# Kernel optimization log

Measured on AMD Instinct MI355X. Metric: run time of the kernel, lower is better.

Reference implementation:

```python
import jax, jax.numpy as jnp
import numpy as np

N, M, E = 20000, 2000, 320000
D_MODEL, HID, HEADS = 128, 128, 4
EPS_BN = 1e-5


def _seg_softmax(a, seg, n):
    # torch_geometric.utils.softmax grouped by seg (here: destination node)
    m = jax.ops.segment_max(a, seg, num_segments=n)
    e = jnp.exp(a - m[seg])
    s = jax.ops.segment_sum(e, seg, num_segments=n)
    return e / (s[seg] + 1e-16)


def _bn(x, g, b):
    # BatchNorm1d, training-mode batch statistics (biased var), affine
    mu = x.mean(0)
    v = x.var(0)
    return (x - mu) * jax.lax.rsqrt(v + EPS_BN) * g + b


def _hconv(x, attr, node_idx, edge_idx, w_edge, lin_w, att, bias, heads):
    # PyG HypergraphConv(use_attention=True, concat=False), dropout off (eval)
    nN, nM = x.shape[0], w_edge.shape[0]
    C = lin_w.shape[1] // heads
    xh = (x @ lin_w).reshape(nN, heads, C)      # node feats per head
    ah = (attr @ lin_w).reshape(nM, heads, C)   # hyperedge feats per head
    x_i = xh[node_idx]                          # [E,H,C] gather per incidence
    a_j = ah[edge_idx]                          # [E,H,C]
    alpha = (x_i * att[:, :C]).sum(-1) + (a_j * att[:, C:]).sum(-1)  # [E,H]
    alpha = jax.nn.leaky_relu(alpha, 0.2)
    alpha = _seg_softmax(alpha, node_idx, nN)
    # D = sum of incident hyperedge weights per node; B = 1/edge_degree * w
    Dd = jax.ops.segment_sum(w_edge[edge_idx], node_idx, num_segments=nN)
    Dinv = jnp.where(Dd > 0, 1.0 / Dd, 0.0)
    Bd = jax.ops.segment_sum(jnp.ones((node_idx.shape[0],), x.dtype), edge_idx, num_segments=nM)
    Binv = jnp.where(Bd > 0, 1.0 / Bd, 0.0) * w_edge
    # node -> hyperedge
    m1 = Binv[edge_idx][:, None, None] * alpha[:, :, None] * x_i
    out_e = jax.ops.segment_sum(m1, edge_idx, num_segments=nM)  # [M,H,C]
    # hyperedge -> node
    m2 = Dinv[node_idx][:, None, None] * alpha[:, :, None] * out_e[edge_idx]
    out_n = jax.ops.segment_sum(m2, node_idx, num_segments=nN)  # [N,H,C]
    return out_n.mean(axis=1) + bias            # concat=False -> head mean


def _forward(x, node_idx, edge_idx, hyperedge_weight, W1, b1, g1, be1,
             lin_w1, att1, bias1, g2, be2, lin_w2, att2, bias2, g3, be3,
             W2, b2, g4, be4):
    nM = hyperedge_weight.shape[0]
    src = x
    h = jax.nn.leaky_relu(x @ W1 + b1, 0.2)
    h = _bn(h, g1, be1)
    # hyperedge_attr = (a.T @ x) == segment_sum of node feats per hyperedge
    attr = jax.ops.segment_sum(h[node_idx], edge_idx, num_segments=nM)
    h = _bn(h + _hconv(h, attr, node_idx, edge_idx, hyperedge_weight,
                       lin_w1, att1, bias1, HEADS), g2, be2)
    attr = jax.ops.segment_sum(h[node_idx], edge_idx, num_segments=nM)
    h = _bn(h + _hconv(h, attr, node_idx, edge_idx, hyperedge_weight,
                       lin_w2, att2, bias2, 1), g3, be3)
    o = jax.nn.leaky_relu(h @ W2 + b2, 0.2)
    return _bn(src + o, g4, be4)


def setup_inputs() -> dict:
    key = jax.random.key(0)
    ks = jax.random.split(key, 12)
    s1 = 1.0 / np.sqrt(D_MODEL)
    s2 = 1.0 / np.sqrt(HID)
    return {
        "x": jax.random.normal(ks[0], (N, D_MODEL), jnp.float32),
        "node_idx": jax.random.randint(ks[1], (E,), 0, N),
        "edge_idx": jax.random.randint(ks[2], (E,), 0, M),
        "hyperedge_weight": jax.random.uniform(ks[3], (M,), jnp.float32, 0.5, 1.5),
        "W1": jax.random.normal(ks[4], (D_MODEL, HID), jnp.float32) * s1,
        "b1": jnp.zeros((HID,), jnp.float32),
        "g1": jnp.ones((HID,), jnp.float32),
        "be1": jnp.zeros((HID,), jnp.float32),
        "lin_w1": jax.random.normal(ks[5], (HID, HEADS * HID), jnp.float32) * s2,
        "att1": jax.random.normal(ks[6], (HEADS, 2 * HID), jnp.float32) * s2,
        "bias1": jnp.zeros((HID,), jnp.float32),
        "g2": jnp.ones((HID,), jnp.float32),
        "be2": jnp.zeros((HID,), jnp.float32),
        "lin_w2": jax.random.normal(ks[7], (HID, HID), jnp.float32) * s2,
        "att2": jax.random.normal(ks[8], (1, 2 * HID), jnp.float32) * s2,
        "bias2": jnp.zeros((HID,), jnp.float32),
        "g3": jnp.ones((HID,), jnp.float32),
        "be3": jnp.zeros((HID,), jnp.float32),
        "W2": jax.random.normal(ks[9], (HID, D_MODEL), jnp.float32) * s2,
        "b2": jnp.zeros((D_MODEL,), jnp.float32),
        "g4": jnp.ones((D_MODEL,), jnp.float32),
        "be4": jnp.zeros((D_MODEL,), jnp.float32),
    }


def reference(x, node_idx, edge_idx, hyperedge_weight, W1, b1, g1, be1,
              lin_w1, att1, bias1, g2, be2, lin_w2, att2, bias2, g3, be3,
              W2, b2, g4, be4):
    return _forward(x, node_idx, edge_idx, hyperedge_weight, W1, b1, g1, be1,
                    lin_w1, att1, bias1, g2, be2, lin_w2, att2, bias2,
                    g3, be3, W2, b2, g4, be4)
```

## Files before the change

### kernel.cpp

```cpp
#include <hip/hip_runtime.h>

#define NN 20000
#define MM 2000
#define EE 320000
static constexpr float SLOPE = 0.2f;
static constexpr float EPSBN = 1e-5f;

__device__ inline float4 f4add(float4 a, float4 b) {
  return make_float4(a.x + b.x, a.y + b.y, a.z + b.z, a.w + b.w);
}
__device__ inline float4 f4fma(float a, float4 v, float4 c) {
  return make_float4(c.x + a * v.x, c.y + a * v.y, c.z + a * v.z, c.w + a * v.w);
}
__device__ inline float leaky(float v) { return (v > 0.f) ? v : SLOPE * v; }

__device__ inline void bn_sc4(const float* __restrict__ st, const float* __restrict__ g,
                              const float* __restrict__ be, float ninv, int c4,
                              float4& sc, float4& sh) {
  float* scp = &sc.x;
  float* shp = &sh.x;
#pragma unroll
  for (int j = 0; j < 4; j++) {
    int c = c4 * 4 + j;
    float mu = st[c] * ninv;
    float var = st[128 + c] * ninv - mu * mu;
    float s = g[c] * rsqrtf(var + EPSBN);
    scp[j] = s;
    shp[j] = be[c] - mu * s;
  }
}

__global__ void k_count(const int* __restrict__ ni, const int* __restrict__ ei,
                        int* ncnt, int* ecnt, int* __restrict__ rank_n,
                        int* __restrict__ rank_e) {
  int e = blockIdx.x * 256 + threadIdx.x;
  if (e >= EE) return;
  rank_n[e] = atomicAdd(&ncnt[ni[e]], 1);
  rank_e[e] = atomicAdd(&ecnt[ei[e]], 1);
}

__global__ __launch_bounds__(1024) void k_scan(const int* __restrict__ cnt,
                                               int* __restrict__ off, int n) {
  __shared__ int swav[16];
  __shared__ int sCarry;
  int t = threadIdx.x;
  int lane = t & 63, wid = t >> 6;
  if (t == 0) sCarry = 0;
  __syncthreads();
  for (int base = 0; base < n; base += 1024) {
    int i = base + t;
    int v = (i < n) ? cnt[i] : 0;
    int x = v;
#pragma unroll
    for (int o = 1; o < 64; o <<= 1) {
      int y = __shfl_up(x, o);
      if (lane >= o) x += y;
    }
    if (lane == 63) swav[wid] = x;
    __syncthreads();
    if (wid == 0) {
      int s = (lane < 16) ? swav[lane] : 0;
#pragma unroll
      for (int o = 1; o < 16; o <<= 1) {
        int y = __shfl_up(s, o);
        if (lane >= o) s += y;
      }
      if (lane < 16) swav[lane] = s;
    }
    __syncthreads();
    int wpre = wid ? swav[wid - 1] : 0;
    int total = swav[15];
    if (i < n) off[i] = sCarry + wpre + x - v;
    __syncthreads();
    if (t == 0) sCarry += total;
    __syncthreads();
  }
  if (t == 0) off[n] = sCarry;
}

__global__ void k_fill(const int* __restrict__ ni, const int* __restrict__ ei,
                       const int* __restrict__ noff, const int* __restrict__ eoff,
                       const int* __restrict__ rank_n, const int* __restrict__ rank_e,
                       int* __restrict__ em_n, int2* __restrict__ npos_e) {
  int e = blockIdx.x * 256 + threadIdx.x;
  if (e >= EE) return;
  int n = ni[e];
  int m = ei[e];
  int pn = noff[n] + rank_n[e];
  int pe = eoff[m] + rank_e[e];
  em_n[pn] = m;
  npos_e[pe] = make_int2(n, pn);
}

__global__ __launch_bounds__(256) void k_gemm128(
    const float* __restrict__ A, const float* __restrict__ W,
    const float* __restrict__ bias, const float* __restrict__ resid,
    const float* __restrict__ st, const float* __restrict__ g,
    const float* __restrict__ be, float ninv, float* __restrict__ out,
    float* __restrict__ stout, int rows) {
  __shared__ float As[32][68];
  __shared__ float Ws[32][132];
  __shared__ float scs[128], shs[128];
  if (st && threadIdx.x < 128) {
    int c = threadIdx.x;
    float mu = st[c] * ninv;
    float var = st[128 + c] * ninv - mu * mu;
    float s = g[c] * rsqrtf(var + EPSBN);
    scs[c] = s;
    shs[c] = be[c] - mu * s;
  }
  if (st) __syncthreads();
  int tx = threadIdx.x & 15, ty = threadIdx.x >> 4;
  int r0 = blockIdx.x * 64;
  float4 acc[4][2];
#pragma unroll
  for (int j = 0; j < 4; j++) acc[j][0] = acc[j][1] = make_float4(0.f, 0.f, 0.f, 0.f);

  for (int k0 = 0; k0 < 128; k0 += 32) {
    __syncthreads();
    {
      int row = threadIdx.x >> 2, kq = threadIdx.x & 3;
      int rr = r0 + row;
      float4 a0 = make_float4(0.f, 0.f, 0.f, 0.f), a1 = a0;
      if (rr < rows) {
        const float* ap = A + (size_t)rr * 128 + k0 + kq * 8;
        a0 = ((const float4*)ap)[0];
        a1 = ((const float4*)ap)[1];
      }
      int kb = k0 + kq * 8;
      if (st) {
        a0.x = a0.x * scs[kb + 0] + shs[kb + 0];
        a0.y = a0.y * scs[kb + 1] + shs[kb + 1];
        a0.z = a0.z * scs[kb + 2] + shs[kb + 2];
        a0.w = a0.w * scs[kb + 3] + shs[kb + 3];
        a1.x = a1.x * scs[kb + 4] + shs[kb + 4];
        a1.y = a1.y * scs[kb + 5] + shs[kb + 5];
        a1.z = a1.z * scs[kb + 6] + shs[kb + 6];
        a1.w = a1.w * scs[kb + 7] + shs[kb + 7];
      }
      int kl = kq * 8;
      As[kl + 0][row] = a0.x;
      As[kl + 1][row] = a0.y;
      As[kl + 2][row] = a0.z;
      As[kl + 3][row] = a0.w;
      As[kl + 4][row] = a1.x;
      As[kl + 5][row] = a1.y;
      As[kl + 6][row] = a1.z;
      As[kl + 7][row] = a1.w;
    }
    {
      int kk = threadIdx.x >> 3, cq = threadIdx.x & 7;
      const float* wp = W + (size_t)(k0 + kk) * 128 + cq * 16;
#pragma unroll
      for (int f = 0; f < 4; f++)
        *(float4*)&Ws[kk][cq * 16 + f * 4] = ((const float4*)wp)[f];
    }
    __syncthreads();
#pragma unroll
    for (int kk = 0; kk < 32; kk++) {
      float4 a = *(const float4*)&As[kk][ty * 4];
      float4 w0 = *(const float4*)&Ws[kk][tx * 8];
      float4 w1 = *(const float4*)&Ws[kk][tx * 8 + 4];
      acc[0][0] = f4fma(a.x, w0, acc[0][0]);
      acc[0][1] = f4fma(a.x, w1, acc[0][1]);
      acc[1][0] = f4fma(a.y, w0, acc[1][0]);
      acc[1][1] = f4fma(a.y, w1, acc[1][1]);
      acc[2][0] = f4fma(a.z, w0, acc[2][0]);
      acc[2][1] = f4fma(a.z, w1, acc[2][1]);
      acc[3][0] = f4fma(a.w, w0, acc[3][0]);
      acc[3][1] = f4fma(a.w, w1, acc[3][1]);
    }
  }
  float4 b0 = ((const float4*)bias)[tx * 2];
  float4 b1 = ((const float4*)bias)[tx * 2 + 1];
  float4 cs0 = make_float4(0.f, 0.f, 0.f, 0.f), cs1 = cs0, cq0 = cs0, cq1 = cs0;
#pragma unroll
  for (int j = 0; j < 4; j++) {
    int r = r0 + ty * 4 + j;
    if (r < rows) {
      float4 o0 = acc[j][0], o1 = acc[j][1];
      o0 = make_float4(leaky(o0.x + b0.x), leaky(o0.y + b0.y), leaky(o0.z + b0.z),
                       leaky(o0.w + b0.w));
      o1 = make_float4(leaky(o1.x + b1.x), leaky(o1.y + b1.y), leaky(o1.z + b1.z),
                       leaky(o1.w + b1.w));
      if (resid) {
        float4 r0v = ((const float4*)resid)[(size_t)r * 32 + tx * 2];
        float4 r1v = ((const float4*)resid)[(size_t)r * 32 + tx * 2 + 1];
        o0 = f4add(o0, r0v);
        o1 = f4add(o1, r1v);
      }
      ((float4*)out)[(size_t)r * 32 + tx * 2] = o0;
      ((float4*)out)[(size_t)r * 32 + tx * 2 + 1] = o1;
      cs0 = f4add(cs0, o0);
      cs1 = f4add(cs1, o1);
      cq0 = make_float4(cq0.x + o0.x * o0.x, cq0.y + o0.y * o0.y, cq0.z + o0.z * o0.z,
                        cq0.w + o0.w * o0.w);
      cq1 = make_float4(cq1.x + o1.x * o1.x, cq1.y + o1.y * o1.y, cq1.z + o1.z * o1.z,
                        cq1.w + o1.w * o1.w);
    }
  }
  __syncthreads();
  float* sumb = &As[0][0];
  float* sqb = &Ws[0][0];
  *(float4*)&sumb[ty * 128 + tx * 8] = cs0;
  *(float4*)&sumb[ty * 128 + tx * 8 + 4] = cs1;
  *(float4*)&sqb[ty * 128 + tx * 8] = cq0;
  *(float4*)&sqb[ty * 128 + tx * 8 + 4] = cq1;
  __syncthreads();
  if (threadIdx.x < 128) {
    float S = 0.f, Q = 0.f;
#pragma unroll
    for (int w = 0; w < 16; w++) {
      S += sumb[w * 128 + threadIdx.x];
      Q += sqb[w * 128 + threadIdx.x];
    }
    atomicAdd(&stout[threadIdx.x], S);
    atomicAdd(&stout[128 + threadIdx.x], Q);
  }
}

template <int H>
__global__ __launch_bounds__(256) void k_oute64(const float* __restrict__ T,
                                                const float* __restrict__ linw,
                                                const int* __restrict__ eoff,
                                                const float* __restrict__ wedge,
                                                float* __restrict__ oute) {
  int h = blockIdx.y;
  __shared__ float As[32][68];
  __shared__ float Ws[32][132];
  int tx = threadIdx.x & 15, ty = threadIdx.x >> 4;
  int r0 = blockIdx.x * 64;
  const float* A = T + (size_t)h * MM * 128;
  float4 acc[4][2];
#pragma unroll
  for (int j = 0; j < 4; j++) acc[j][0] = acc[j][1] = make_float4(0.f, 0.f, 0.f, 0.f);

  for (int k0 = 0; k0 < 128; k0 += 32) {
    __syncthreads();
    {
      int row = threadIdx.x >> 2, kq = threadIdx.x & 3;
      int rr = r0 + row;
      float4 a0 = make_float4(0.f, 0.f, 0.f, 0.f), a1 = a0;
      if (rr < MM) {
        const float* ap = A + (size_t)rr * 128 + k0 + kq * 8;
        a0 = ((const float4*)ap)[0];
        a1 = ((const float4*)ap)[1];
      }
      int kb = kq * 8;
      As[kb + 0][row] = a0.x;
      As[kb + 1][row] = a0.y;
      As[kb + 2][row] = a0.z;
      As[kb + 3][row] = a0.w;
      As[kb + 4][row] = a1.x;
      As[kb + 5][row] = a1.y;
      As[kb + 6][row] = a1.z;
      As[kb + 7][row] = a1.w;
    }
    {
      int kk = threadIdx.x >> 3, cq = threadIdx.x & 7;
      const float* wp = linw + (size_t)(k0 + kk) * (128 * H) + h * 128 + cq * 16;
#pragma unroll
      for (int f = 0; f < 4; f++)
        *(float4*)&Ws[kk][cq * 16 + f * 4] = ((const float4*)wp)[f];
    }
    __syncthreads();
#pragma unroll
    for (int kk = 0; kk < 32; kk++) {
      float4 a = *(const float4*)&As[kk][ty * 4];
      float4 w0 = *(const float4*)&Ws[kk][tx * 8];
      float4 w1 = *(const float4*)&Ws[kk][tx * 8 + 4];
      acc[0][0] = f4fma(a.x, w0, acc[0][0]);
      acc[0][1] = f4fma(a.x, w1, acc[0][1]);
      acc[1][0] = f4fma(a.y, w0, acc[1][0]);
      acc[1][1] = f4fma(a.y, w1, acc[1][1]);
      acc[2][0] = f4fma(a.z, w0, acc[2][0]);
      acc[2][1] = f4fma(a.z, w1, acc[2][1]);
      acc[3][0] = f4fma(a.w, w0, acc[3][0]);
      acc[3][1] = f4fma(a.w, w1, acc[3][1]);
    }
  }
#pragma unroll
  for (int j = 0; j < 4; j++) {
    int m = r0 + ty * 4 + j;
    if (m >= MM) break;
    int d = eoff[m + 1] - eoff[m];
    float bv = (d > 0) ? wedge[m] / (float)d : 0.f;
    float4 o0 = acc[j][0], o1 = acc[j][1];
    o0 = make_float4(bv * o0.x, bv * o0.y, bv * o0.z, bv * o0.w);
    o1 = make_float4(bv * o1.x, bv * o1.y, bv * o1.z, bv * o1.w);
    ((float4*)oute)[((size_t)m * H + h) * 32 + tx * 2] = o0;
    ((float4*)oute)[((size_t)m * H + h) * 32 + tx * 2 + 1] = o1;
  }
}

__global__ __launch_bounds__(256) void k_colstats(const float4* __restrict__ X4,
                                                  int rows, float* __restrict__ st) {
  int c4 = threadIdx.x & 31, rs = threadIdx.x >> 5, wid = threadIdx.x >> 6;
  int r0 = blockIdx.x * 256;
  int rend = min(r0 + 256, rows);
  float4 s = make_float4(0.f, 0.f, 0.f, 0.f), q = s;
  for (int r = r0 + rs; r < rend; r += 8) {
    float4 v = X4[(size_t)r * 32 + c4];
    s = f4add(s, v);
    q = make_float4(q.x + v.x * v.x, q.y + v.y * v.y, q.z + v.z * v.z, q.w + v.w * v.w);
  }
  s.x += __shfl_xor(s.x, 32); s.y += __shfl_xor(s.y, 32);
  s.z += __shfl_xor(s.z, 32); s.w += __shfl_xor(s.w, 32);
  q.x += __shfl_xor(q.x, 32); q.y += __shfl_xor(q.y, 32);
  q.z += __shfl_xor(q.z, 32); q.w += __shfl_xor(q.w, 32);
  __shared__ float4 red[4][32][2];
  if ((threadIdx.x & 63) < 32) {
    red[wid][c4][0] = s;
    red[wid][c4][1] = q;
  }
  __syncthreads();
  if (threadIdx.x < 32) {
    float4 S = f4add(f4add(red[0][threadIdx.x][0], red[1][threadIdx.x][0]),
                     f4add(red[2][threadIdx.x][0], red[3][threadIdx.x][0]));
    float4 Q = f4add(f4add(red[0][threadIdx.x][1], red[1][threadIdx.x][1]),
                     f4add(red[2][threadIdx.x][1], red[3][threadIdx.x][1]));
    int c = threadIdx.x * 4;
    atomicAdd(&st[c + 0], S.x);
    atomicAdd(&st[c + 1], S.y);
    atomicAdd(&st[c + 2], S.z);
    atomicAdd(&st[c + 3], S.w);
    atomicAdd(&st[128 + c + 0], Q.x);
    atomicAdd(&st[128 + c + 1], Q.y);
    atomicAdd(&st[128 + c + 2], Q.z);
    atomicAdd(&st[128 + c + 3], Q.w);
  }
}

__global__ void k_bnapply_final(const float4* __restrict__ X4,
                                const float* __restrict__ st,
                                const float* __restrict__ g,
                                const float* __restrict__ be, float ninv,
                                float4* __restrict__ Y4, int total4) {
  int i = blockIdx.x * 256 + threadIdx.x;
  if (i >= total4) return;
  int c4 = i & 31;
  float4 sc, sh;
  bn_sc4(st, g, be, ninv, c4, sc, sh);
  float4 v = X4[i];
  Y4[i] = make_float4(v.x * sc.x + sh.x, v.y * sc.y + sh.y, v.z * sc.z + sh.z,
                      v.w * sc.w + sh.w);
}

template <int H>
__global__ void k_uv(const float* __restrict__ linw, const float* __restrict__ att,
                     float* __restrict__ UVT) {
  int idx = blockIdx.x * 256 + threadIdx.x;
  if (idx >= 128 * H) return;
  int h = idx >> 7, k = idx & 127;
  float u = 0.f, v = 0.f;
  for (int c = 0; c < 128; c++) {
    float w = linw[(size_t)k * (128 * H) + h * 128 + c];
    u += w * att[h * 256 + c];
    v += w * att[h * 256 + 128 + c];
  }
  UVT[h * 128 + k] = u;
  UVT[(H + h) * 128 + k] = v;
}

template <int H>
__global__ void k_dots(const float4* __restrict__ X4, int rows,
                       const float* __restrict__ UVT, const float* __restrict__ st,
                       const float* __restrict__ g, const float* __restrict__ be,
                       float ninv, float* __restrict__ dotx, float* __restrict__ hv) {
  __shared__ float4 Ut[2 * H * 32];
  __shared__ float4 scl[32], shl[32];
  if (threadIdx.x < 32) {
    float4 sc, sh;
    bn_sc4(st, g, be, ninv, threadIdx.x, sc, sh);
    scl[threadIdx.x] = sc;
    shl[threadIdx.x] = sh;
  }
  for (int i = threadIdx.x; i < 2 * H * 32; i += 256) Ut[i] = ((const float4*)UVT)[i];
  __syncthreads();
  int idx = blockIdx.x * 256 + threadIdx.x;
  if (idx >= rows * 2 * H) return;
  int n = idx / (2 * H), h2 = idx - n * (2 * H);
  const float4* xr = X4 + (size_t)n * 32;
  const float4* ur = Ut + h2 * 32;
  float s = 0.f;
#pragma unroll 8
  for (int q = 0; q < 32; q++) {
    float4 a = xr[q], b = ur[q], c = scl[q], d = shl[q];
    float ax = a.x * c.x + d.x, ay = a.y * c.y + d.y;
    float az = a.z * c.z + d.z, aw = a.w * c.w + d.w;
    s += ax * b.x + ay * b.y + az * b.z + aw * b.w;
  }
  if (h2 < H)
    dotx[n * H + h2] = s;
  else
    hv[n * H + (h2 - H)] = s;
}

template <int H>
__global__ void k_dota(const float* __restrict__ hv, const int* __restrict__ eoff,
                       const int2* __restrict__ npos_e, float* __restrict__ dota) {
  int lane = threadIdx.x & 63;
  int m = blockIdx.x * 4 + (threadIdx.x >> 6);
  int s = eoff[m], t = eoff[m + 1];
  if (H == 4) {
    float4 acc = make_float4(0.f, 0.f, 0.f, 0.f);
    const float4* hv4 = (const float4*)hv;
    for (int j = s + lane; j < t; j += 64) acc = f4add(acc, hv4[npos_e[j].x]);
#pragma unroll
    for (int o = 32; o >= 1; o >>= 1) {
      acc.x += __shfl_xor(acc.x, o);
      acc.y += __shfl_xor(acc.y, o);
      acc.z += __shfl_xor(acc.z, o);
      acc.w += __shfl_xor(acc.w, o);
    }
    if (lane == 0) ((float4*)dota)[m] = acc;
  } else {
    float acc = 0.f;
    for (int j = s + lane; j < t; j += 64) acc += hv[npos_e[j].x];
#pragma unroll
    for (int o = 32; o >= 1; o >>= 1) acc += __shfl_xor(acc, o);
    if (lane == 0) dota[m] = acc;
  }
}

template <int H>
__global__ void k_softmax(const int* __restrict__ noff, const int* __restrict__ em_n,
                          const float* __restrict__ dotx, const float* __restrict__ dota,
                          const float* __restrict__ wedge, float* __restrict__ alpha,
                          float* __restrict__ Dinv) {
  int lane = threadIdx.x & 63;
  int n = blockIdx.x * 4 + (threadIdx.x >> 6);
  int s = noff[n], t = noff[n + 1];
  int deg = t - s;
  int h = lane & (H - 1);
  float dx = dotx[n * H + h];
  if (deg <= 64) {
    int em0 = 0;
    float dd = 0.f;
    if (lane < deg) {
      em0 = em_n[s + lane];
      dd = wedge[em0];
    }
#pragma unroll
    for (int o = 32; o >= 1; o >>= 1) dd += __shfl_xor(dd, o);
    if (lane == 0) Dinv[n] = (dd > 0.f) ? 1.f / dd : 0.f;

    constexpr int KMAX = (H == 4) ? 4 : 1;
    int P = deg * H;
    float vc[KMAX];
    float mx = -3.0e38f;
#pragma unroll
    for (int k = 0; k < KMAX; k++) {
      int p = lane + 64 * k;
      int idx = (H == 4) ? (p >> 2) : p;
      int em = __shfl(em0, idx);
      float v = dx + dota[em * H + h];
      v = leaky(v);
      vc[k] = v;
      if (p < P) mx = fmaxf(mx, v);
    }
#pragma unroll
    for (int o = H; o < 64; o <<= 1) mx = fmaxf(mx, __shfl_xor(mx, o));
    float sm = 0.f;
#pragma unroll
    for (int k = 0; k < KMAX; k++) {
      int p = lane + 64 * k;
      float e = __expf(vc[k] - mx);
      vc[k] = e;
      if (p < P) sm += e;
    }
#pragma unroll
    for (int o = H; o < 64; o <<= 1) sm += __shfl_xor(sm, o);
    float inv = 1.f / (sm + 1e-16f);
#pragma unroll
    for (int k = 0; k < KMAX; k++) {
      int p = lane + 64 * k;
      if (p < P) alpha[s * H + p] = vc[k] * inv;
    }
  } else {
    float dd = 0.f;
    for (int i = s + lane; i < t; i += 64) dd += wedge[em_n[i]];
#pragma unroll
    for (int o = 32; o >= 1; o >>= 1) dd += __shfl_xor(dd, o);
    if (lane == 0) Dinv[n] = (dd > 0.f) ? 1.f / dd : 0.f;
    int P = deg * H;
    float mx = -3.0e38f;
    for (int p = lane; p < P; p += 64) {
      int i = s + ((H == 4) ? (p >> 2) : p);
      float v = leaky(dx + dota[em_n[i] * H + h]);
      mx = fmaxf(mx, v);
    }
#pragma unroll
    for (int o = H; o < 64; o <<= 1) mx = fmaxf(mx, __shfl_xor(mx, o));
    float sm = 0.f;
    for (int p = lane; p < P; p += 64) {
      int i = s + ((H == 4) ? (p >> 2) : p);
      float v = leaky(dx + dota[em_n[i] * H + h]);
      sm += __expf(v - mx);
    }
#pragma unroll
    for (int o = H; o < 64; o <<= 1) sm += __shfl_xor(sm, o);
    float inv = 1.f / (sm + 1e-16f);
    for (int p = lane; p < P; p += 64) {
      int i = s + ((H == 4) ? (p >> 2) : p);
      float v = leaky(dx + dota[em_n[i] * H + h]);
      alpha[s * H + p] = __expf(v - mx) * inv;
    }
  }
}

template <int H>
__global__ __launch_bounds__(256) void k_T(const float4* __restrict__ h4raw,
                                           const int* __restrict__ eoff,
                                           const int2* __restrict__ npos_e,
                                           const float* __restrict__ alpha,
                                           const float* __restrict__ st,
                                           const float* __restrict__ g,
                                           const float* __restrict__ be, float ninv,
                                           float4* __restrict__ T4) {
  int m = blockIdx.x;
  int slot = threadIdx.x >> 5, c = threadIdx.x & 31;
  int wv = threadIdx.x >> 6;
  int s = eoff[m], t = eoff[m + 1];
  __shared__ int sofs[256];
  __shared__ float sal[256 * H];
  __shared__ float4 red[4][H][32];
  __shared__ float4 redA[4];
  __shared__ float sAsum[4];
  float4 acc[H];
#pragma unroll
  for (int hh = 0; hh < H; hh++) acc[hh] = make_float4(0.f, 0.f, 0.f, 0.f);
  float4 asum = make_float4(0.f, 0.f, 0.f, 0.f);

  for (int c0 = s; c0 < t; c0 += 256) {
    int cnt = min(256, t - c0);
    __syncthreads();
    if (threadIdx.x < cnt) {
      int2 np = npos_e[c0 + threadIdx.x];
      sofs[threadIdx.x] = np.x * 32;
      if (H == 4) {
        float4 a4 = ((const float4*)alpha)[np.y];
        ((float4*)sal)[threadIdx.x] = a4;
        asum = f4add(asum, a4);
      } else {
        float a = alpha[np.y];
        sal[threadIdx.x] = a;
        asum.x += a;
      }
    }
    __syncthreads();
#pragma unroll 4
    for (int j = slot; j < cnt; j += 8) {
      int ofs = sofs[j];
      float4 v = h4raw[(size_t)ofs + c];
      if (H == 4) {
        float4 a4 = ((const float4*)sal)[j];
        acc[0] = f4fma(a4.x, v, acc[0]);
        acc[1 % H] = f4fma(a4.y, v, acc[1 % H]);
        acc[2 % H] = f4fma(a4.z, v, acc[2 % H]);
        acc[3 % H] = f4fma(a4.w, v, acc[3 % H]);
      } else {
        acc[0] = f4fma(sal[j], v, acc[0]);
      }
    }
  }
#pragma unroll
  for (int hh = 0; hh < H; hh++) {
    float4 a = acc[hh];
    a.x += __shfl_xor(a.x, 32); a.y += __shfl_xor(a.y, 32);
    a.z += __shfl_xor(a.z, 32); a.w += __shfl_xor(a.w, 32);
    acc[hh] = a;
  }
#pragma unroll
  for (int o = 32; o >= 1; o >>= 1) {
    asum.x += __shfl_xor(asum.x, o); asum.y += __shfl_xor(asum.y, o);
    asum.z += __shfl_xor(asum.z, o); asum.w += __shfl_xor(asum.w, o);
  }
  if ((threadIdx.x & 63) < 32) {
#pragma unroll
    for (int hh = 0; hh < H; hh++) red[wv][hh][c] = acc[hh];
  }
  if ((threadIdx.x & 63) == 0) redA[wv] = asum;
  __syncthreads();
  if (threadIdx.x == 0) {
    float4 A = f4add(f4add(redA[0], redA[1]), f4add(redA[2], redA[3]));
    sAsum[0] = A.x; sAsum[1] = A.y; sAsum[2] = A.z; sAsum[3] = A.w;
  }
  __syncthreads();
  if (threadIdx.x < 32 * H) {
    int hh = threadIdx.x >> 5, cc = threadIdx.x & 31;
    float4 r = f4add(f4add(red[0][hh][cc], red[1][hh][cc]),
                     f4add(red[2][hh][cc], red[3][hh][cc]));
    float as = sAsum[hh];
    float4 sc, sh;
    bn_sc4(st, g, be, ninv, cc, sc, sh);
    r = make_float4(sc.x * r.x + sh.x * as, sc.y * r.y + sh.y * as,
                    sc.z * r.z + sh.z * as, sc.w * r.w + sh.w * as);
    T4[((size_t)hh * MM + m) * 32 + cc] = r;
  }
}

template <int H>
__global__ __launch_bounds__(256) void k_phase9(
    const int* __restrict__ noff, const int* __restrict__ em_n,
    const float* __restrict__ alpha, const float4* __restrict__ oute4,
    const float* __restrict__ Dinv, const float* __restrict__ bias,
    const float4* __restrict__ hres4, const float* __restrict__ st,
    const float* __restrict__ g, const float* __restrict__ be, float ninv,
    float4* __restrict__ out4) {
  int wv = threadIdx.x >> 6, lane = threadIdx.x & 63;
  int n = blockIdx.x * 4 + wv;
  int slot = lane >> 5, c = lane & 31;
  int s = noff[n], t = noff[n + 1];
  int deg = t - s;
  float4 acc = make_float4(0.f, 0.f, 0.f, 0.f);
  if (deg <= 64) {
    int m_l = 0;
    float4 a_l = make_float4(0.f, 0.f, 0.f, 0.f);
    if (lane < deg) {
      m_l = em_n[s + lane];
      if (H == 4)
        a_l = ((const float4*)alpha)[s + lane];
      else
        a_l.x = alpha[s + lane];
    }
    for (int i = slot; i < deg; i += 2) {
      int m = __shfl(m_l, i);
      if (H == 4) {
        float ax = __shfl(a_l.x, i), ay = __shfl(a_l.y, i);
        float az = __shfl(a_l.z, i), aw = __shfl(a_l.w, i);
        const float4* base = oute4 + (size_t)m * 128 + c;
        acc = f4fma(ax, base[0], acc);
        acc = f4fma(ay, base[32], acc);
        acc = f4fma(az, base[64], acc);
        acc = f4fma(aw, base[96], acc);
      } else {
        float a = __shfl(a_l.x, i);
        acc = f4fma(a, oute4[(size_t)m * 32 + c], acc);
      }
    }
  } else {
    for (int i = s + slot; i < t; i += 2) {
      int m = em_n[i];
      if (H == 4) {
        float4 a4 = ((const float4*)alpha)[i];
        const float4* base = oute4 + (size_t)m * 128 + c;
        acc = f4fma(a4.x, base[0], acc);
        acc = f4fma(a4.y, base[32], acc);
        acc = f4fma(a4.z, base[64], acc);
        acc = f4fma(a4.w, base[96], acc);
      } else {
        acc = f4fma(alpha[i], oute4[(size_t)m * 32 + c], acc);
      }
    }
  }
  acc.x += __shfl_xor(acc.x, 32); acc.y += __shfl_xor(acc.y, 32);
  acc.z += __shfl_xor(acc.z, 32); acc.w += __shfl_xor(acc.w, 32);
  if (slot == 0) {
    float scn = Dinv[n] * (1.f / H);
    float4 scB, shB;
    bn_sc4(st, g, be, ninv, c, scB, shB);
    float4 hr = hres4[(size_t)n * 32 + c];
    hr = make_float4(hr.x * scB.x + shB.x, hr.y * scB.y + shB.y, hr.z * scB.z + shB.z,
                     hr.w * scB.w + shB.w);
    float4 bi = ((const float4*)bias)[c];
    out4[(size_t)n * 32 + c] =
        make_float4(hr.x + scn * acc.x + bi.x, hr.y + scn * acc.y + bi.y,
                    hr.z + scn * acc.z + bi.z, hr.w + scn * acc.w + bi.w);
  }
}

static inline size_t alignup(size_t x) { return (x + 255) & ~(size_t)255; }

extern "C" void kernel_launch(void* const* d_in, const int* in_sizes, int n_in,
                              void* d_out, int out_size, void* d_ws, size_t ws_size,
                              hipStream_t stream) {
  const float* x = (const float*)d_in[0];
  const int* node_idx = (const int*)d_in[1];
  const int* edge_idx = (const int*)d_in[2];
  const float* wedge = (const float*)d_in[3];
  const float* W1 = (const float*)d_in[4];
  const float* b1 = (const float*)d_in[5];
  const float* g1 = (const float*)d_in[6];
  const float* be1 = (const float*)d_in[7];
  const float* linw1 = (const float*)d_in[8];
  const float* att1 = (const float*)d_in[9];
  const float* bias1 = (const float*)d_in[10];
  const float* g2 = (const float*)d_in[11];
  const float* be2 = (const float*)d_in[12];
  const float* linw2 = (const float*)d_in[13];
  const float* att2 = (const float*)d_in[14];
  const float* bias2 = (const float*)d_in[15];
  const float* g3 = (const float*)d_in[16];
  const float* be3 = (const float*)d_in[17];
  const float* W2 = (const float*)d_in[18];
  const float* b2 = (const float*)d_in[19];
  const float* g4 = (const float*)d_in[20];
  const float* be4 = (const float*)d_in[21];
  float* out = (float*)d_out;

  char* ws = (char*)d_ws;
  size_t off = 0;
  auto alloc = [&](size_t bytes) -> void* {
    void* p = ws + off;
    off = alignup(off + bytes);
    return p;
  };
  float* buf0 = (float*)alloc((size_t)NN * 128 * 4);
  float* buf1 = (float*)alloc((size_t)NN * 128 * 4);
  float* Tbuf = (float*)alloc((size_t)4 * MM * 128 * 4);
  float* oute = (float*)alloc((size_t)MM * 4 * 128 * 4);
  float* alpha = (float*)alloc((size_t)EE * 4 * 4);
  float* dotx = (float*)alloc((size_t)NN * 4 * 4);
  float* hv = (float*)alloc((size_t)NN * 4 * 4);
  float* dota = (float*)alloc((size_t)MM * 4 * 4);
  float* UVT = (float*)alloc(128 * 8 * 4);
  float* Dinv = (float*)alloc((size_t)NN * 4);
  int* noff = (int*)alloc((size_t)(NN + 1) * 4);
  int* eoff = (int*)alloc((size_t)(MM + 1) * 4);
  int* em_n = (int*)alloc((size_t)EE * 4);
  int2* npos_e = (int2*)alloc((size_t)EE * 8);
  int* rank_n = (int*)alloc((size_t)EE * 4);
  int* rank_e = (int*)alloc((size_t)EE * 4);
  size_t zero_bytes = ((size_t)(NN + MM) + 4 * 256) * 4;
  int* zero_region = (int*)alloc(zero_bytes);
  int* ncnt = zero_region;
  int* ecnt = ncnt + NN;
  float* bnst = (float*)(ecnt + MM);
  (void)ws_size;
  (void)in_sizes;
  (void)n_in;
  (void)out_size;

  (void)hipMemsetAsync(zero_region, 0, zero_bytes, stream);

  k_count<<<(EE + 255) / 256, 256, 0, stream>>>(node_idx, edge_idx, ncnt, ecnt,
                                                rank_n, rank_e);
  k_scan<<<1, 1024, 0, stream>>>(ncnt, noff, NN);
  k_scan<<<1, 1024, 0, stream>>>(ecnt, eoff, MM);
  k_fill<<<(EE + 255) / 256, 256, 0, stream>>>(node_idx, edge_idx, noff, eoff, rank_n,
                                               rank_e, em_n, npos_e);

  const float ninv = 1.f / (float)NN;
  const int gemm_grid = (NN + 63) / 64;
  const int cs_grid = (NN + 255) / 256;
  float* st0 = bnst + 0 * 256;
  float* st1 = bnst + 1 * 256;
  float* st2 = bnst + 2 * 256;
  float* st3 = bnst + 3 * 256;

  k_gemm128<<<gemm_grid, 256, 0, stream>>>(x, W1, b1, nullptr, nullptr, nullptr,
                                           nullptr, 0.f, buf0, st0, NN);

  k_uv<4><<<2, 256, 0, stream>>>(linw1, att1, UVT);
  k_dots<4><<<(NN * 8 + 255) / 256, 256, 0, stream>>>((const float4*)buf0, NN, UVT,
                                                      st0, g1, be1, ninv, dotx, hv);
  k_dota<4><<<MM / 4, 256, 0, stream>>>(hv, eoff, npos_e, dota);
  k_softmax<4><<<NN / 4, 256, 0, stream>>>(noff, em_n, dotx, dota, wedge, alpha, Dinv);
  k_T<4><<<MM, 256, 0, stream>>>((const float4*)buf0, eoff, npos_e, alpha, st0, g1,
                                 be1, ninv, (float4*)Tbuf);
  {
    dim3 g((MM + 63) / 64, 4);
    k_oute64<4><<<g, 256, 0, stream>>>(Tbuf, linw1, eoff, wedge, oute);
  }
  k_phase9<4><<<NN / 4, 256, 0, stream>>>(noff, em_n, alpha, (const float4*)oute, Dinv,
                                          bias1, (const float4*)buf0, st0, g1, be1,
                                          ninv, (float4*)buf1);
  k_colstats<<<cs_grid, 256, 0, stream>>>((const float4*)buf1, NN, st1);

  k_uv<1><<<1, 256, 0, stream>>>(linw2, att2, UVT);
  k_dots<1><<<(NN * 2 + 255) / 256, 256, 0, stream>>>((const float4*)buf1, NN, UVT,
                                                      st1, g2, be2, ninv, dotx, hv);
  k_dota<1><<<MM / 4, 256, 0, stream>>>(hv, eoff, npos_e, dota);
  k_softmax<1><<<NN / 4, 256, 0, stream>>>(noff, em_n, dotx, dota, wedge, alpha, Dinv);
  k_T<1><<<MM, 256, 0, stream>>>((const float4*)buf1, eoff, npos_e, alpha, st1, g2,
                                 be2, ninv, (float4*)Tbuf);
  {
    dim3 g((MM + 63) / 64, 1);
    k_oute64<1><<<g, 256, 0, stream>>>(Tbuf, linw2, eoff, wedge, oute);
  }
  k_phase9<1><<<NN / 4, 256, 0, stream>>>(noff, em_n, alpha, (const float4*)oute, Dinv,
                                          bias2, (const float4*)buf1, st1, g2, be2,
                                          ninv, (float4*)buf0);
  k_colstats<<<cs_grid, 256, 0, stream>>>((const float4*)buf0, NN, st2);

  k_gemm128<<<gemm_grid, 256, 0, stream>>>(buf0, W2, b2, x, st2, g3, be3, ninv, buf1,
                                           st3, NN);
  k_bnapply_final<<<(NN * 32 + 255) / 256, 256, 0, stream>>>(
      (const float4*)buf1, st3, g4, be4, ninv, (float4*)out, NN * 32);
}
```

Baseline: 351.0 us.

## Slice incidence counters to cut atomic contention and merge small setup kernels

The per-node and per-hyperedge counting atomics are spread over 8 slices keyed by block index. This is meant to reduce contention on hot counters, especially the 2000 hyperedge counters that each receive about 160 increments. A new slice-scan kernel turns the slice counts into per-slice offsets and totals, and the two single-block scans are merged into one two-block launch. The two attention-projection kernels are also fused into one launch placed at the start. The cost is a larger memset, one extra kernel, and extra reads of the slice offsets in the fill kernel.

After: 315.6 us. -10.1%, faster.

```diff
diff --git a/kernel.cpp b/kernel.cpp
--- a/kernel.cpp
+++ b/kernel.cpp
@@ -3,6 +3,7 @@
 #define NN 20000
 #define MM 2000
 #define EE 320000
+#define NSLICE 8
 static constexpr float SLOPE = 0.2f;
 static constexpr float EPSBN = 1e-5f;
 
@@ -31,16 +32,47 @@
 }
 
 __global__ void k_count(const int* __restrict__ ni, const int* __restrict__ ei,
-                        int* ncnt, int* ecnt, int* __restrict__ rank_n,
+                        int* cntN, int* cntE, int* __restrict__ rank_n,
                         int* __restrict__ rank_e) {
   int e = blockIdx.x * 256 + threadIdx.x;
   if (e >= EE) return;
-  rank_n[e] = atomicAdd(&ncnt[ni[e]], 1);
-  rank_e[e] = atomicAdd(&ecnt[ei[e]], 1);
-}
-
-__global__ __launch_bounds__(1024) void k_scan(const int* __restrict__ cnt,
-                                               int* __restrict__ off, int n) {
+  int s = blockIdx.x & (NSLICE - 1);
+  rank_n[e] = atomicAdd(&cntN[s * NN + ni[e]], 1);
+  rank_e[e] = atomicAdd(&cntE[s * MM + ei[e]], 1);
+}
+
+__global__ void k_slicescan(int* __restrict__ cntN, int* __restrict__ totN,
+                            int* __restrict__ cntE, int* __restrict__ totE) {
+  int i = blockIdx.x * 256 + threadIdx.x;
+  if (i < NN) {
+    int run = 0;
+#pragma unroll
+    for (int s = 0; s < NSLICE; s++) {
+      int t = cntN[s * NN + i];
+      cntN[s * NN + i] = run;
+      run += t;
+    }
+    totN[i] = run;
+  } else if (i < NN + MM) {
+    int m = i - NN;
+    int run = 0;
+#pragma unroll
+    for (int s = 0; s < NSLICE; s++) {
+      int t = cntE[s * MM + m];
+      cntE[s * MM + m] = run;
+      run += t;
+    }
+    totE[m] = run;
+  }
+}
+
+__global__ __launch_bounds__(1024) void k_scan2(const int* __restrict__ cntA,
+                                                int* __restrict__ offA, int nA,
+                                                const int* __restrict__ cntB,
+                                                int* __restrict__ offB, int nB) {
+  const int* cnt = blockIdx.x ? cntB : cntA;
+  int* off = blockIdx.x ? offB : offA;
+  int n = blockIdx.x ? nB : nA;
   __shared__ int swav[16];
   __shared__ int sCarry;
   int t = threadIdx.x;
@@ -80,14 +112,16 @@
 
 __global__ void k_fill(const int* __restrict__ ni, const int* __restrict__ ei,
                        const int* __restrict__ noff, const int* __restrict__ eoff,
+                       const int* __restrict__ cntN, const int* __restrict__ cntE,
                        const int* __restrict__ rank_n, const int* __restrict__ rank_e,
                        int* __restrict__ em_n, int2* __restrict__ npos_e) {
   int e = blockIdx.x * 256 + threadIdx.x;
   if (e >= EE) return;
+  int s = blockIdx.x & (NSLICE - 1);
   int n = ni[e];
   int m = ei[e];
-  int pn = noff[n] + rank_n[e];
-  int pe = eoff[m] + rank_e[e];
+  int pn = noff[n] + cntN[s * NN + n] + rank_n[e];
+  int pe = eoff[m] + cntE[s * MM + m] + rank_e[e];
   em_n[pn] = m;
   npos_e[pe] = make_int2(n, pn);
 }
@@ -346,20 +380,33 @@
                       v.w * sc.w + sh.w);
 }
 
-template <int H>
-__global__ void k_uv(const float* __restrict__ linw, const float* __restrict__ att,
-                     float* __restrict__ UVT) {
-  int idx = blockIdx.x * 256 + threadIdx.x;
-  if (idx >= 128 * H) return;
-  int h = idx >> 7, k = idx & 127;
-  float u = 0.f, v = 0.f;
-  for (int c = 0; c < 128; c++) {
-    float w = linw[(size_t)k * (128 * H) + h * 128 + c];
-    u += w * att[h * 256 + c];
-    v += w * att[h * 256 + 128 + c];
-  }
-  UVT[h * 128 + k] = u;
-  UVT[(H + h) * 128 + k] = v;
+__global__ void k_uv_all(const float* __restrict__ linw1, const float* __restrict__ att1,
+                         float* __restrict__ UVT1, const float* __restrict__ linw2,
+                         const float* __restrict__ att2, float* __restrict__ UVT2) {
+  if (blockIdx.x < 2) {
+    constexpr int H = 4;
+    int idx = blockIdx.x * 256 + threadIdx.x;
+    int h = idx >> 7, k = idx & 127;
+    float u = 0.f, v = 0.f;
+    for (int c = 0; c < 128; c++) {
+      float w = linw1[(size_t)k * (128 * H) + h * 128 + c];
+      u += w * att1[h * 256 + c];
+      v += w * att1[h * 256 + 128 + c];
+    }
+    UVT1[h * 128 + k] = u;
+    UVT1[(H + h) * 128 + k] = v;
+  } else {
+    if (threadIdx.x >= 128) return;
+    int k = threadIdx.x;
+    float u = 0.f, v = 0.f;
+    for (int c = 0; c < 128; c++) {
+      float w = linw2[(size_t)k * 128 + c];
+      u += w * att2[c];
+      v += w * att2[128 + c];
+    }
+    UVT2[k] = u;
+    UVT2[128 + k] = v;
+  }
 }
 
 template <int H>
@@ -714,7 +761,8 @@
   float* dotx = (float*)alloc((size_t)NN * 4 * 4);
   float* hv = (float*)alloc((size_t)NN * 4 * 4);
   float* dota = (float*)alloc((size_t)MM * 4 * 4);
-  float* UVT = (float*)alloc(128 * 8 * 4);
+  float* UVT1 = (float*)alloc(128 * 8 * 4);
+  float* UVT2 = (float*)alloc(128 * 2 * 4);
   float* Dinv = (float*)alloc((size_t)NN * 4);
   int* noff = (int*)alloc((size_t)(NN + 1) * 4);
   int* eoff = (int*)alloc((size_t)(MM + 1) * 4);
@@ -722,11 +770,13 @@
   int2* npos_e = (int2*)alloc((size_t)EE * 8);
   int* rank_n = (int*)alloc((size_t)EE * 4);
   int* rank_e = (int*)alloc((size_t)EE * 4);
-  size_t zero_bytes = ((size_t)(NN + MM) + 4 * 256) * 4;
+  int* totN = (int*)alloc((size_t)NN * 4);
+  int* totE = (int*)alloc((size_t)MM * 4);
+  size_t zero_bytes = ((size_t)NSLICE * (NN + MM) + 4 * 256) * 4;
   int* zero_region = (int*)alloc(zero_bytes);
-  int* ncnt = zero_region;
-  int* ecnt = ncnt + NN;
-  float* bnst = (float*)(ecnt + MM);
+  int* cntN = zero_region;
+  int* cntE = cntN + NSLICE * NN;
+  float* bnst = (float*)(cntE + NSLICE * MM);
   (void)ws_size;
   (void)in_sizes;
   (void)n_in;
@@ -734,12 +784,14 @@
 
   (void)hipMemsetAsync(zero_region, 0, zero_bytes, stream);
 
-  k_count<<<(EE + 255) / 256, 256, 0, stream>>>(node_idx, edge_idx, ncnt, ecnt,
+  k_uv_all<<<3, 256, 0, stream>>>(linw1, att1, UVT1, linw2, att2, UVT2);
+
+  k_count<<<(EE + 255) / 256, 256, 0, stream>>>(node_idx, edge_idx, cntN, cntE,
                                                 rank_n, rank_e);
-  k_scan<<<1, 1024, 0, stream>>>(ncnt, noff, NN);
-  k_scan<<<1, 1024, 0, stream>>>(ecnt, eoff, MM);
-  k_fill<<<(EE + 255) / 256, 256, 0, stream>>>(node_idx, edge_idx, noff, eoff, rank_n,
-                                               rank_e, em_n, npos_e);
+  k_slicescan<<<(NN + MM + 255) / 256, 256, 0, stream>>>(cntN, totN, cntE, totE);
+  k_scan2<<<2, 1024, 0, stream>>>(totN, noff, NN, totE, eoff, MM);
+  k_fill<<<(EE + 255) / 256, 256, 0, stream>>>(node_idx, edge_idx, noff, eoff, cntN,
+                                               cntE, rank_n, rank_e, em_n, npos_e);
 
   const float ninv = 1.f / (float)NN;
   const int gemm_grid = (NN + 63) / 64;
@@ -752,8 +804,7 @@
   k_gemm128<<<gemm_grid, 256, 0, stream>>>(x, W1, b1, nullptr, nullptr, nullptr,
                                            nullptr, 0.f, buf0, st0, NN);
 
-  k_uv<4><<<2, 256, 0, stream>>>(linw1, att1, UVT);
-  k_dots<4><<<(NN * 8 + 255) / 256, 256, 0, stream>>>((const float4*)buf0, NN, UVT,
+  k_dots<4><<<(NN * 8 + 255) / 256, 256, 0, stream>>>((const float4*)buf0, NN, UVT1,
                                                       st0, g1, be1, ninv, dotx, hv);
   k_dota<4><<<MM / 4, 256, 0, stream>>>(hv, eoff, npos_e, dota);
   k_softmax<4><<<NN / 4, 256, 0, stream>>>(noff, em_n, dotx, dota, wedge, alpha, Dinv);
@@ -768,8 +819,7 @@
                                           ninv, (float4*)buf1);
   k_colstats<<<cs_grid, 256, 0, stream>>>((const float4*)buf1, NN, st1);
 
-  k_uv<1><<<1, 256, 0, stream>>>(linw2, att2, UVT);
-  k_dots<1><<<(NN * 2 + 255) / 256, 256, 0, stream>>>((const float4*)buf1, NN, UVT,
+  k_dots<1><<<(NN * 2 + 255) / 256, 256, 0, stream>>>((const float4*)buf1, NN, UVT2,
                                                       st1, g2, be2, ninv, dotx, hv);
   k_dota<1><<<MM / 4, 256, 0, stream>>>(hv, eoff, npos_e, dota);
   k_softmax<1><<<NN / 4, 256, 0, stream>>>(noff, em_n, dotx, dota, wedge, alpha, Dinv);
```
